# Performance work log

Hardware: AMD Instinct MI355X
Metric: run time of the kernel (lower is better)

Reference implementation:

```python
import jax, jax.numpy as jnp
import numpy as np

N_NODES = 50000
N_EDGES = 640000
D_IN, D_HID, D_OUT = 128, 256, 2


def setup_inputs() -> dict:
    key = jax.random.key(0)
    ks = jax.random.split(key, 8)
    node_features = jax.random.normal(ks[0], (N_NODES, D_IN), dtype=jnp.float32)
    src = jax.random.randint(ks[1], (N_EDGES,), 0, N_NODES)
    dst = jax.random.randint(ks[2], (N_EDGES,), 0, N_NODES)
    s_in = 1.0 / np.sqrt(D_IN)
    s_hid = 1.0 / np.sqrt(D_HID)
    return {
        "node_features": node_features,
        "src": src,
        "dst": dst,
        "W1_self": jax.random.normal(ks[3], (D_IN, D_HID), dtype=jnp.float32) * s_in,
        "W1_neigh": jax.random.normal(ks[4], (D_IN, D_HID), dtype=jnp.float32) * s_in,
        "b1": jnp.zeros((D_HID,), dtype=jnp.float32),
        "W2_self": jax.random.normal(ks[5], (D_HID, D_OUT), dtype=jnp.float32) * s_hid,
        "W2_neigh": jax.random.normal(ks[6], (D_HID, D_OUT), dtype=jnp.float32) * s_hid,
        "b2": jnp.zeros((D_OUT,), dtype=jnp.float32),
    }


def _sage_mean(x, src, dst, W_self, W_neigh, b, n_nodes):
    # gather source-node features along edges, mean-reduce into destinations
    msg = x[src]                                                  # [E, D]
    agg = jax.ops.segment_sum(msg, dst, num_segments=n_nodes)     # [N, D]
    deg = jax.ops.segment_sum(jnp.ones((src.shape[0], 1), x.dtype), dst,
                              num_segments=n_nodes)               # [N, 1]
    h_neigh = agg / jnp.maximum(deg, 1.0)
    return x @ W_self + h_neigh @ W_neigh + b


def reference(node_features, src, dst, W1_self, W1_neigh, b1, W2_self, W2_neigh, b2):
    h = _sage_mean(node_features, src, dst, W1_self, W1_neigh, b1, N_NODES)
    h = jax.nn.relu(h)
    logits = _sage_mean(h, src, dst, W2_self, W2_neigh, b2, N_NODES)
    return logits
```

## Files before the change

### kernel.cpp

```cpp
#include <hip/hip_runtime.h>

#define D_IN 128
#define D_HID 256
#define CH 1024
#define MPAD 50048

typedef short bf16x8 __attribute__((ext_vector_type(8)));
typedef float f32x4 __attribute__((ext_vector_type(4)));
typedef float f32x16 __attribute__((ext_vector_type(16)));
typedef unsigned short ushort8 __attribute__((ext_vector_type(8)));

#define AS1 __attribute__((address_space(1)))
#define AS3 __attribute__((address_space(3)))

__device__ __forceinline__ unsigned short f2bf_rne(float x) {
  unsigned int u = __float_as_uint(x);
  unsigned int r = (u + 0x7FFFu + ((u >> 16) & 1u)) >> 16;
  return (unsigned short)r;
}
__device__ __forceinline__ float bf2f(unsigned short b) {
  return __uint_as_float(((unsigned int)b) << 16);
}

__global__ void k_hist(const int* __restrict__ dst, int* __restrict__ deg, int E) {
  int e = blockIdx.x * blockDim.x + threadIdx.x;
  if (e < E) atomicAdd(&deg[dst[e]], 1);
}

__global__ __launch_bounds__(256) void k_csum(const int* __restrict__ deg,
                                              int* __restrict__ csum, int n) {
  __shared__ int ws[4];
  int t = threadIdx.x, lane = t & 63, w = t >> 6;
  int base = blockIdx.x * CH + t * 4;
  int s = 0;
  #pragma unroll
  for (int j = 0; j < 4; ++j) { int i = base + j; s += (i < n) ? deg[i] : 0; }
  #pragma unroll
  for (int off = 32; off > 0; off >>= 1) s += __shfl_down(s, off, 64);
  if (lane == 0) ws[w] = s;
  __syncthreads();
  if (t == 0) csum[blockIdx.x] = ws[0] + ws[1] + ws[2] + ws[3];
}

__global__ void k_coff(const int* __restrict__ csum, int* __restrict__ coff, int nb) {
  int lane = threadIdx.x & 63;
  int v = (lane < nb) ? csum[lane] : 0;
  int x = v;
  #pragma unroll
  for (int off = 1; off < 64; off <<= 1) {
    int u = __shfl_up(x, off, 64);
    if (lane >= off) x += u;
  }
  if (lane < nb) coff[lane] = x - v;
}

__global__ __launch_bounds__(256) void k_scanw(const int* __restrict__ deg,
                                               const int* __restrict__ coff,
                                               int* __restrict__ rs, int n) {
  __shared__ int ws[4];
  int t = threadIdx.x, lane = t & 63, w = t >> 6;
  int base = blockIdx.x * CH + t * 4;
  int d[4];
  #pragma unroll
  for (int j = 0; j < 4; ++j) { int i = base + j; d[j] = (i < n) ? deg[i] : 0; }
  int tt = d[0] + d[1] + d[2] + d[3];
  int x = tt;
  #pragma unroll
  for (int off = 1; off < 64; off <<= 1) {
    int u = __shfl_up(x, off, 64);
    if (lane >= off) x += u;
  }
  if (lane == 63) ws[w] = x;
  __syncthreads();
  if (t == 0) { int s = 0;
    #pragma unroll
    for (int j = 0; j < 4; ++j) { int tmp = ws[j]; ws[j] = s; s += tmp; } }
  __syncthreads();
  int excl = ws[w] + (x - tt) + coff[blockIdx.x];
  #pragma unroll
  for (int j = 0; j < 4; ++j) {
    int i = base + j;
    excl += d[j];
    if (i < n) rs[i + 1] = excl;
  }
  if (blockIdx.x == 0 && t == 0) rs[0] = 0;
}

__global__ void k_scatter(const int* __restrict__ src, const int* __restrict__ dst,
                          const int* __restrict__ rs, int* __restrict__ cursor,
                          int* __restrict__ esrc, int E) {
  int e = blockIdx.x * blockDim.x + threadIdx.x;
  if (e < E) {
    int d = dst[e];
    int pos = rs[d] + atomicAdd(&cursor[d], 1);
    esrc[pos] = src[e];
  }
}

__global__ __launch_bounds__(256) void k_convW(const float* __restrict__ W1s,
                                               const float* __restrict__ W1n,
                                               unsigned short* __restrict__ Bth,
                                               unsigned short* __restrict__ Btl) {
  int k = blockIdx.x;
  int col = threadIdx.x;
  float w = (k < 128) ? W1s[(size_t)k * D_HID + col]
                      : W1n[(size_t)(k - 128) * D_HID + col];
  unsigned short hi = f2bf_rne(w);
  unsigned short lo = f2bf_rne(w - bf2f(hi));
  Bth[(size_t)col * 256 + k] = hi;
  Btl[(size_t)col * 256 + k] = lo;
}

__global__ void k_agg1(const float* __restrict__ X, const int* __restrict__ rs,
                       const int* __restrict__ esrc,
                       unsigned short* __restrict__ Mh,
                       unsigned short* __restrict__ Ml, int n) {
  int wid = (blockIdx.x * blockDim.x + threadIdx.x) >> 6;
  int lane = threadIdx.x & 63;
  if (wid >= n) return;
  int s0 = rs[wid], s1 = rs[wid + 1];
  float ax0 = 0.f, ay0 = 0.f, ax1 = 0.f, ay1 = 0.f;
  int e = s0;
  for (; e + 3 < s1; e += 4) {
    int i0 = esrc[e + 0], i1 = esrc[e + 1], i2 = esrc[e + 2], i3 = esrc[e + 3];
    float2 v0 = *(const float2*)(X + (size_t)i0 * D_IN + lane * 2);
    float2 v1 = *(const float2*)(X + (size_t)i1 * D_IN + lane * 2);
    float2 v2 = *(const float2*)(X + (size_t)i2 * D_IN + lane * 2);
    float2 v3 = *(const float2*)(X + (size_t)i3 * D_IN + lane * 2);
    ax0 += v0.x; ay0 += v0.y;
    ax1 += v1.x; ay1 += v1.y;
    ax0 += v2.x; ay0 += v2.y;
    ax1 += v3.x; ay1 += v3.y;
  }
  for (; e < s1; ++e) {
    int s = esrc[e];
    float2 v = *(const float2*)(X + (size_t)s * D_IN + lane * 2);
    ax0 += v.x; ay0 += v.y;
  }
  int d = s1 - s0;
  float inv = 1.0f / (float)(d > 1 ? d : 1);
  float mx = (ax0 + ax1) * inv, my = (ay0 + ay1) * inv;
  unsigned short hx = f2bf_rne(mx), hy = f2bf_rne(my);
  unsigned short lx = f2bf_rne(mx - bf2f(hx)), ly = f2bf_rne(my - bf2f(hy));
  *(ushort2*)(Mh + (size_t)wid * 128 + lane * 2) = make_ushort2(hx, hy);
  *(ushort2*)(Ml + (size_t)wid * 128 + lane * 2) = make_ushort2(lx, ly);
}

__global__ __launch_bounds__(256, 3) void k_gemm1(
    const float* __restrict__ X,
    const unsigned short* __restrict__ Mh, const unsigned short* __restrict__ Ml,
    const unsigned short* __restrict__ Bth, const unsigned short* __restrict__ Btl,
    const float* __restrict__ b1, const float* __restrict__ W2s,
    const float* __restrict__ W2n, float* __restrict__ SP, int n) {
  __shared__ __align__(16) unsigned short sA[2][2][2][512];
  __shared__ __align__(16) unsigned short sB[8][2][2][512];

  const int tid = threadIdx.x;
  const int w = tid >> 6;
  const int l = tid & 63;
  const int wm = w & 1, wn = w >> 1;
  const int r32 = l & 31;
  const int kh = l >> 5;
  const int m0 = blockIdx.x * 64;

  f32x16 acc[4];
  #pragma unroll
  for (int q = 0; q < 4; ++q) acc[q] = (f32x16)0.f;

  const int sm = w & 1, sk = w >> 1;
  const int arow = m0 + sm * 32 + r32;
  const int xrow = (arow < n) ? arow : (n - 1);

  for (int ks = 0; ks < 8; ++ks) {
    const int kt = ks * 32;
    if (kt < 128) {
      const float* src = X + (size_t)xrow * D_IN + kt + sk * 16 + kh * 8;
      float4 u0 = *(const float4*)(src);
      float4 u1 = *(const float4*)(src + 4);
      float v[8] = {u0.x, u0.y, u0.z, u0.w, u1.x, u1.y, u1.z, u1.w};
      ushort8 hh, ll;
      #pragma unroll
      for (int i = 0; i < 8; ++i) {
        unsigned short h = f2bf_rne(v[i]);
        hh[i] = h;
        ll[i] = f2bf_rne(v[i] - bf2f(h));
      }
      *(ushort8*)(&sA[sm][sk][0][l * 8]) = hh;
      *(ushort8*)(&sA[sm][sk][1][l * 8]) = ll;
    } else {
      const unsigned short* mh = Mh + (size_t)arow * 128 + (kt - 128) + sk * 16 + kh * 8;
      const unsigned short* ml = Ml + (size_t)arow * 128 + (kt - 128) + sk * 16 + kh * 8;
      __builtin_amdgcn_global_load_lds((AS1 const void*)mh, (AS3 void*)&sA[sm][sk][0][0], 16, 0, 0);
      __builtin_amdgcn_global_load_lds((AS1 const void*)ml, (AS3 void*)&sA[sm][sk][1][0], 16, 0, 0);
    }
    #pragma unroll
    for (int q = 0; q < 2; ++q) {
      int ct = w * 2 + q;
      #pragma unroll
      for (int kstep = 0; kstep < 2; ++kstep) {
        const unsigned short* bh = Bth + (size_t)(ct * 32 + r32) * 256 + kt + kstep * 16 + kh * 8;
        const unsigned short* bl = Btl + (size_t)(ct * 32 + r32) * 256 + kt + kstep * 16 + kh * 8;
        __builtin_amdgcn_global_load_lds((AS1 const void*)bh, (AS3 void*)&sB[ct][kstep][0][0], 16, 0, 0);
        __builtin_amdgcn_global_load_lds((AS1 const void*)bl, (AS3 void*)&sB[ct][kstep][1][0], 16, 0, 0);
      }
    }
    __syncthreads();

    #pragma unroll
    for (int kstep = 0; kstep < 2; ++kstep) {
      bf16x8 ah = *(const bf16x8*)(&sA[wm][kstep][0][l * 8]);
      bf16x8 al = *(const bf16x8*)(&sA[wm][kstep][1][l * 8]);
      #pragma unroll
      for (int q = 0; q < 4; ++q) {
        int ct = wn * 4 + q;
        bf16x8 bh = *(const bf16x8*)(&sB[ct][kstep][0][l * 8]);
        bf16x8 bl = *(const bf16x8*)(&sB[ct][kstep][1][l * 8]);
        acc[q] = __builtin_amdgcn_mfma_f32_32x32x16_bf16(ah, bh, acc[q], 0, 0, 0);
        acc[q] = __builtin_amdgcn_mfma_f32_32x32x16_bf16(ah, bl, acc[q], 0, 0, 0);
        acc[q] = __builtin_amdgcn_mfma_f32_32x32x16_bf16(al, bh, acc[q], 0, 0, 0);
      }
    }
    __syncthreads();
  }

  float b1v[4]; float2 w2sv[4], w2nv[4];
  #pragma unroll
  for (int q = 0; q < 4; ++q) {
    int col = wn * 128 + q * 32 + r32;
    b1v[q] = b1[col];
    w2sv[q] = *(const float2*)(W2s + (size_t)col * 2);
    w2nv[q] = *(const float2*)(W2n + (size_t)col * 2);
  }
  float4* fpart = (float4*)&sB[0][0][0][0];
  #pragma unroll
  for (int j = 0; j < 16; ++j) {
    float s0 = 0.f, s1 = 0.f, p0 = 0.f, p1 = 0.f;
    #pragma unroll
    for (int q = 0; q < 4; ++q) {
      float h = fmaxf(acc[q][j] + b1v[q], 0.f);
      s0 += h * w2sv[q].x; s1 += h * w2sv[q].y;
      p0 += h * w2nv[q].x; p1 += h * w2nv[q].y;
    }
    #pragma unroll
    for (int off = 1; off < 32; off <<= 1) {
      s0 += __shfl_xor(s0, off, 64);
      s1 += __shfl_xor(s1, off, 64);
      p0 += __shfl_xor(p0, off, 64);
      p1 += __shfl_xor(p1, off, 64);
    }
    if (r32 == 0) {
      int row = wm * 32 + (j & 3) + 8 * (j >> 2) + 4 * kh;
      float4 o; o.x = s0; o.y = s1; o.z = p0; o.w = p1;
      fpart[wn * 64 + row] = o;
    }
  }
  __syncthreads();
  if (w == 0) {
    float4 a = fpart[l], b = fpart[64 + l];
    float4 o; o.x = a.x + b.x; o.y = a.y + b.y; o.z = a.z + b.z; o.w = a.w + b.w;
    *(float4*)(SP + (size_t)(m0 + l) * 4) = o;
  }
}

__global__ void k_agg2(const float* __restrict__ SP,
                       const int* __restrict__ rs, const int* __restrict__ esrc,
                       const float* __restrict__ b2,
                       float* __restrict__ out, int n) {
  int nid = blockIdx.x * blockDim.x + threadIdx.x;
  if (nid >= n) return;
  int s0 = rs[nid], s1 = rs[nid + 1];
  float a00 = 0.f, a01 = 0.f, a10 = 0.f, a11 = 0.f;
  int e = s0;
  for (; e + 3 < s1; e += 4) {
    int i0 = esrc[e + 0], i1 = esrc[e + 1], i2 = esrc[e + 2], i3 = esrc[e + 3];
    float2 p0 = *(const float2*)(SP + (size_t)i0 * 4 + 2);
    float2 p1 = *(const float2*)(SP + (size_t)i1 * 4 + 2);
    float2 p2 = *(const float2*)(SP + (size_t)i2 * 4 + 2);
    float2 p3 = *(const float2*)(SP + (size_t)i3 * 4 + 2);
    a00 += p0.x; a01 += p0.y;
    a10 += p1.x; a11 += p1.y;
    a00 += p2.x; a01 += p2.y;
    a10 += p3.x; a11 += p3.y;
  }
  for (; e < s1; ++e) {
    int s = esrc[e];
    float2 p = *(const float2*)(SP + (size_t)s * 4 + 2);
    a00 += p.x; a01 += p.y;
  }
  int d = s1 - s0;
  float inv = 1.0f / (float)(d > 1 ? d : 1);
  float2 sv = *(const float2*)(SP + (size_t)nid * 4);
  float2 o;
  o.x = sv.x + b2[0] + (a00 + a10) * inv;
  o.y = sv.y + b2[1] + (a01 + a11) * inv;
  *(float2*)(out + (size_t)nid * 2) = o;
}

extern "C" void kernel_launch(void* const* d_in, const int* in_sizes, int n_in,
                              void* d_out, int out_size, void* d_ws, size_t ws_size,
                              hipStream_t stream) {
  const float* X   = (const float*)d_in[0];
  const int*   src = (const int*)d_in[1];
  const int*   dst = (const int*)d_in[2];
  const float* W1s = (const float*)d_in[3];
  const float* W1n = (const float*)d_in[4];
  const float* b1  = (const float*)d_in[5];
  const float* W2s = (const float*)d_in[6];
  const float* W2n = (const float*)d_in[7];
  const float* b2  = (const float*)d_in[8];
  float* out = (float*)d_out;

  const int N = in_sizes[0] / D_IN;
  const int E = in_sizes[1];
  const int NB = (N + CH - 1) / CH;

  int* deg    = (int*)d_ws;
  int* cursor = deg + N;
  int* rs     = cursor + N;
  int* csum   = rs + (N + 8);
  int* coff   = csum + 64;
  int* esrc   = coff + 64;
  float* SP   = (float*)(esrc + E);
  unsigned short* Mh  = (unsigned short*)(SP + (size_t)MPAD * 4);
  unsigned short* Ml  = Mh + (size_t)MPAD * 128;
  unsigned short* Bth = Ml + (size_t)MPAD * 128;
  unsigned short* Btl = Bth + 256 * 256;

  hipMemsetAsync(deg, 0, sizeof(int) * (size_t)2 * N, stream);

  int eb = (E + 255) / 256;
  k_convW  <<<256, 256, 0, stream>>>(W1s, W1n, Bth, Btl);
  k_hist   <<<eb, 256, 0, stream>>>(dst, deg, E);
  k_csum   <<<NB, 256, 0, stream>>>(deg, csum, N);
  k_coff   <<<1, 64, 0, stream>>>(csum, coff, NB);
  k_scanw  <<<NB, 256, 0, stream>>>(deg, coff, rs, N);
  k_scatter<<<eb, 256, 0, stream>>>(src, dst, rs, cursor, esrc, E);
  k_agg1   <<<(N + 3) / 4, 256, 0, stream>>>(X, rs, esrc, Mh, Ml, N);
  k_gemm1  <<<MPAD / 64, 256, 0, stream>>>(X, Mh, Ml, Bth, Btl,
                                           b1, W2s, W2n, SP, N);
  k_agg2   <<<(N + 255) / 256, 256, 0, stream>>>(SP, rs, esrc, b2, out, N);
}
```

Baseline: 255.7 us.

## Fuse init kernels and replace three-pass scan with single-pass decoupled lookback

Merges the memset of the degree and cursor arrays and the weight bf16 hi/lo split into one init kernel. The same kernel also zeroes the new scan state. The three-kernel prefix sum (block sums, block offsets, final scan) becomes one kernel that takes dynamic block ids and uses a decoupled lookback over per-block status flags. This removes several launches and the dependency bubbles between them. In exchange, one thread per block serially spins on flags, and correctness now depends on atomic memory ordering.

```diff
diff --git a/kernel.cpp b/kernel.cpp
--- a/kernel.cpp
+++ b/kernel.cpp
@@ -2,7 +2,6 @@
 
 #define D_IN 128
 #define D_HID 256
-#define CH 1024
 #define MPAD 50048
 
 typedef short bf16x8 __attribute__((ext_vector_type(8)));
@@ -22,68 +21,80 @@
   return __uint_as_float(((unsigned int)b) << 16);
 }
 
+__global__ __launch_bounds__(256) void k_init(
+    const float* __restrict__ W1s, const float* __restrict__ W1n,
+    int* __restrict__ deg, int* __restrict__ cursor,
+    unsigned int* __restrict__ bstate, int* __restrict__ vcount,
+    unsigned short* __restrict__ Bth, unsigned short* __restrict__ Btl, int N) {
+  int g = blockIdx.x * 256 + threadIdx.x;
+  if (g < N) { deg[g] = 0; cursor[g] = 0; }
+  if (g < 256) bstate[g] = 0u;
+  if (g == 0) *vcount = 0;
+  int k = g >> 8;
+  int col = g & 255;
+  float w = (k < 128) ? W1s[(size_t)k * D_HID + col]
+                      : W1n[(size_t)(k - 128) * D_HID + col];
+  unsigned short hi = f2bf_rne(w);
+  unsigned short lo = f2bf_rne(w - bf2f(hi));
+  Bth[(size_t)col * 256 + k] = hi;
+  Btl[(size_t)col * 256 + k] = lo;
+}
+
 __global__ void k_hist(const int* __restrict__ dst, int* __restrict__ deg, int E) {
   int e = blockIdx.x * blockDim.x + threadIdx.x;
   if (e < E) atomicAdd(&deg[dst[e]], 1);
 }
 
-__global__ __launch_bounds__(256) void k_csum(const int* __restrict__ deg,
-                                              int* __restrict__ csum, int n) {
+__global__ __launch_bounds__(256) void k_scan(const int* __restrict__ deg,
+                                              int* __restrict__ rs,
+                                              unsigned int* __restrict__ bstate,
+                                              int* __restrict__ vcount, int n) {
   __shared__ int ws[4];
-  int t = threadIdx.x, lane = t & 63, w = t >> 6;
-  int base = blockIdx.x * CH + t * 4;
-  int s = 0;
-  #pragma unroll
-  for (int j = 0; j < 4; ++j) { int i = base + j; s += (i < n) ? deg[i] : 0; }
-  #pragma unroll
-  for (int off = 32; off > 0; off >>= 1) s += __shfl_down(s, off, 64);
-  if (lane == 0) ws[w] = s;
-  __syncthreads();
-  if (t == 0) csum[blockIdx.x] = ws[0] + ws[1] + ws[2] + ws[3];
-}
-
-__global__ void k_coff(const int* __restrict__ csum, int* __restrict__ coff, int nb) {
-  int lane = threadIdx.x & 63;
-  int v = (lane < nb) ? csum[lane] : 0;
+  __shared__ int sbid, stotal, sprefix;
+  if (threadIdx.x == 0) sbid = atomicAdd(vcount, 1);
+  __syncthreads();
+  const int bid = sbid;
+  const int tid = threadIdx.x;
+  const int lane = tid & 63, wv = tid >> 6;
+  const int i = bid * 256 + tid;
+  int v = (i < n) ? deg[i] : 0;
   int x = v;
   #pragma unroll
   for (int off = 1; off < 64; off <<= 1) {
     int u = __shfl_up(x, off, 64);
     if (lane >= off) x += u;
   }
-  if (lane < nb) coff[lane] = x - v;
-}
-
-__global__ __launch_bounds__(256) void k_scanw(const int* __restrict__ deg,
-                                               const int* __restrict__ coff,
-                                               int* __restrict__ rs, int n) {
-  __shared__ int ws[4];
-  int t = threadIdx.x, lane = t & 63, w = t >> 6;
-  int base = blockIdx.x * CH + t * 4;
-  int d[4];
-  #pragma unroll
-  for (int j = 0; j < 4; ++j) { int i = base + j; d[j] = (i < n) ? deg[i] : 0; }
-  int tt = d[0] + d[1] + d[2] + d[3];
-  int x = tt;
-  #pragma unroll
-  for (int off = 1; off < 64; off <<= 1) {
-    int u = __shfl_up(x, off, 64);
-    if (lane >= off) x += u;
-  }
-  if (lane == 63) ws[w] = x;
-  __syncthreads();
-  if (t == 0) { int s = 0;
-    #pragma unroll
-    for (int j = 0; j < 4; ++j) { int tmp = ws[j]; ws[j] = s; s += tmp; } }
-  __syncthreads();
-  int excl = ws[w] + (x - tt) + coff[blockIdx.x];
-  #pragma unroll
-  for (int j = 0; j < 4; ++j) {
-    int i = base + j;
-    excl += d[j];
-    if (i < n) rs[i + 1] = excl;
-  }
-  if (blockIdx.x == 0 && t == 0) rs[0] = 0;
+  if (lane == 63) ws[wv] = x;
+  __syncthreads();
+  if (tid == 0) { int s = 0;
+    #pragma unroll
+    for (int j = 0; j < 4; ++j) { int t = ws[j]; ws[j] = s; s += t; } }
+  __syncthreads();
+  const int incl = x + ws[wv];
+  if (tid == 255) {
+    stotal = incl;
+    __hip_atomic_store(&bstate[bid], (1u << 30) | (unsigned)incl,
+                       __ATOMIC_RELEASE, __HIP_MEMORY_SCOPE_AGENT);
+  }
+  __syncthreads();
+  if (tid == 0) {
+    int prefix = 0;
+    for (int j = bid - 1; j >= 0; --j) {
+      unsigned s;
+      do {
+        s = __hip_atomic_load(&bstate[j], __ATOMIC_ACQUIRE,
+                              __HIP_MEMORY_SCOPE_AGENT);
+      } while ((s >> 30) == 0u);
+      prefix += (int)(s & 0x3FFFFFFFu);
+      if ((s >> 30) == 2u) break;
+    }
+    sprefix = prefix;
+    __hip_atomic_store(&bstate[bid], (2u << 30) | (unsigned)(prefix + stotal),
+                       __ATOMIC_RELEASE, __HIP_MEMORY_SCOPE_AGENT);
+  }
+  __syncthreads();
+  if (i < n) rs[i + 1] = incl + sprefix;
+  if (bid == 0 && tid == 0) rs[0] = 0;
 }
 
 __global__ void k_scatter(const int* __restrict__ src, const int* __restrict__ dst,
@@ -95,20 +106,6 @@
     int pos = rs[d] + atomicAdd(&cursor[d], 1);
     esrc[pos] = src[e];
   }
-}
-
-__global__ __launch_bounds__(256) void k_convW(const float* __restrict__ W1s,
-                                               const float* __restrict__ W1n,
-                                               unsigned short* __restrict__ Bth,
-                                               unsigned short* __restrict__ Btl) {
-  int k = blockIdx.x;
-  int col = threadIdx.x;
-  float w = (k < 128) ? W1s[(size_t)k * D_HID + col]
-                      : W1n[(size_t)(k - 128) * D_HID + col];
-  unsigned short hi = f2bf_rne(w);
-  unsigned short lo = f2bf_rne(w - bf2f(hi));
-  Bth[(size_t)col * 256 + k] = hi;
-  Btl[(size_t)col * 256 + k] = lo;
 }
 
 __global__ void k_agg1(const float* __restrict__ X, const int* __restrict__ rs,
@@ -174,9 +171,9 @@
   for (int ks = 0; ks < 8; ++ks) {
     const int kt = ks * 32;
     if (kt < 128) {
-      const float* src = X + (size_t)xrow * D_IN + kt + sk * 16 + kh * 8;
-      float4 u0 = *(const float4*)(src);
-      float4 u1 = *(const float4*)(src + 4);
+      const float* srcx = X + (size_t)xrow * D_IN + kt + sk * 16 + kh * 8;
+      float4 u0 = *(const float4*)(srcx);
+      float4 u1 = *(const float4*)(srcx + 4);
       float v[8] = {u0.x, u0.y, u0.z, u0.w, u1.x, u1.y, u1.z, u1.w};
       ushort8 hh, ll;
       #pragma unroll
@@ -312,28 +309,25 @@
 
   const int N = in_sizes[0] / D_IN;
   const int E = in_sizes[1];
-  const int NB = (N + CH - 1) / CH;
 
   int* deg    = (int*)d_ws;
   int* cursor = deg + N;
   int* rs     = cursor + N;
-  int* csum   = rs + (N + 8);
-  int* coff   = csum + 64;
-  int* esrc   = coff + 64;
+  unsigned int* bstate = (unsigned int*)(rs + (N + 8));
+  int* vcount = (int*)(bstate + 256);
+  int* esrc   = vcount + 16;
   float* SP   = (float*)(esrc + E);
   unsigned short* Mh  = (unsigned short*)(SP + (size_t)MPAD * 4);
   unsigned short* Ml  = Mh + (size_t)MPAD * 128;
   unsigned short* Bth = Ml + (size_t)MPAD * 128;
   unsigned short* Btl = Bth + 256 * 256;
 
-  hipMemsetAsync(deg, 0, sizeof(int) * (size_t)2 * N, stream);
-
   int eb = (E + 255) / 256;
-  k_convW  <<<256, 256, 0, stream>>>(W1s, W1n, Bth, Btl);
+  int sb = (N + 255) / 256;
+  k_init   <<<256, 256, 0, stream>>>(W1s, W1n, deg, cursor, bstate, vcount,
+                                     Bth, Btl, N);
   k_hist   <<<eb, 256, 0, stream>>>(dst, deg, E);
-  k_csum   <<<NB, 256, 0, stream>>>(deg, csum, N);
-  k_coff   <<<1, 64, 0, stream>>>(csum, coff, NB);
-  k_scanw  <<<NB, 256, 0, stream>>>(deg, coff, rs, N);
+  k_scan   <<<sb, 256, 0, stream>>>(deg, rs, bstate, vcount, N);
   k_scatter<<<eb, 256, 0, stream>>>(src, dst, rs, cursor, esrc, E);
   k_agg1   <<<(N + 3) / 4, 256, 0, stream>>>(X, rs, esrc, Mh, Ml, N);
   k_gemm1  <<<MPAD / 64, 256, 0, stream>>>(X, Mh, Ml, Bth, Btl,
```

New measurement: 289.1 us. 13.1% more time.
